# Kernel optimization log

Hardware: AMD Instinct MI355X
Metric: run time of the kernel (lower is better)

The kernel has to match this reference:

```python
import jax, jax.numpy as jnp
import numpy as np
from jax import lax

B, N, NPOINT = 8, 8192, 1024
NSAMPLE = (16, 32)
IN_CH = 64
MLPS = ((64, 64, 128), (64, 96, 128))
EPS = 1e-5


def setup_inputs() -> dict:
    key = jax.random.key(0)
    ks = jax.random.split(key, 16)
    inp = {}
    inp["xyz"] = jax.random.normal(ks[0], (B, 3, N), jnp.float32)
    inp["points"] = jax.random.normal(ks[1], (B, IN_CH, N), jnp.float32)
    ki = 2
    for i, mlp in enumerate(MLPS):
        last = IN_CH + 3
        for j, out in enumerate(mlp):
            inp["w%d_%d" % (i, j)] = jax.random.normal(ks[ki], (out, last), jnp.float32) * (1.0 / float(np.sqrt(last)))
            inp["b%d_%d" % (i, j)] = jnp.zeros((out,), jnp.float32)
            inp["g%d_%d" % (i, j)] = jnp.ones((out,), jnp.float32)
            inp["be%d_%d" % (i, j)] = jnp.zeros((out,), jnp.float32)
            ki += 1
            last = out
    return inp


def _fps(xyz_t):
    # farthest point sampling; xyz_t: [B, N, 3] -> [B, NPOINT] int32
    Bb, Nn, _ = xyz_t.shape

    def step(carry, _):
        dist, far = carry
        c = jnp.take_along_axis(xyz_t, far[:, None, None], axis=1)  # [B,1,3]
        d = jnp.sum((xyz_t - c) ** 2, -1)
        dist = jnp.minimum(dist, d)
        return (dist, jnp.argmax(dist, -1).astype(jnp.int32)), far

    init = (jnp.full((Bb, Nn), 1e10, jnp.float32), jnp.zeros((Bb,), jnp.int32))
    _, cent = lax.scan(step, init, None, length=NPOINT)
    return cent.T  # [B, NPOINT]


def _gather(p, idx):
    # p: [B, N, C], idx: [B, ...] -> [B, ..., C]
    return jax.vmap(lambda a, i: a[i])(p, idx)


def _sqdist(a, b):
    # a: [B, S, 3], b: [B, N, 3] -> [B, S, N] squared euclidean distance
    return (jnp.sum(a * a, -1)[:, :, None] + jnp.sum(b * b, -1)[:, None, :]
            - 2.0 * jnp.einsum('bsc,bnc->bsn', a, b))


def _mlp(x, params):
    # x: [B, C, S, K]; 1x1 Conv2d + BatchNorm2d (batch stats, training mode) + ReLU
    for w, b, g, be in params:
        x = jnp.einsum('oc,bcsk->bosk', w, x) + b[None, :, None, None]
        m = x.mean((0, 2, 3), keepdims=True)
        v = x.var((0, 2, 3), keepdims=True)
        x = (x - m) * lax.rsqrt(v + EPS) * g[None, :, None, None] + be[None, :, None, None]
        x = jax.nn.relu(x)
    return x


def _forward(xyz, points, params):
    xyz_t = jnp.transpose(xyz, (0, 2, 1))     # [B, N, 3]
    pts_t = jnp.transpose(points, (0, 2, 1))  # [B, N, C]
    fps_idx = _fps(xyz_t)
    new_xyz = _gather(xyz_t, fps_idx)         # [B, S, 3]
    outs = []
    for i, k in enumerate(NSAMPLE):
        d = _sqdist(new_xyz, xyz_t)           # [B, S, N]
        _, idx = lax.top_k(-d, k)             # k nearest neighbors
        g_xyz = _gather(xyz_t, idx) - new_xyz[:, :, None, :]  # [B, S, k, 3]
        g_pts = _gather(pts_t, idx)                           # [B, S, k, C]
        feat = jnp.transpose(jnp.concatenate([g_xyz, g_pts], -1), (0, 3, 1, 2))  # [B, 3+C, S, k]
        outs.append(jnp.max(_mlp(feat, params[i]), -1))       # [B, C_out, S]
    return jnp.transpose(new_xyz, (0, 2, 1)), jnp.concatenate(outs, 1)


def reference(xyz, points, w0_0, b0_0, g0_0, be0_0, w0_1, b0_1, g0_1, be0_1, w0_2, b0_2, g0_2, be0_2, w1_0, b1_0, g1_0, be1_0, w1_1, b1_1, g1_1, be1_1, w1_2, b1_2, g1_2, be1_2):
    params = [[(w0_0, b0_0, g0_0, be0_0), (w0_1, b0_1, g0_1, be0_1), (w0_2, b0_2, g0_2, be0_2)],
              [(w1_0, b1_0, g1_0, be1_0), (w1_1, b1_1, g1_1, be1_1), (w1_2, b1_2, g1_2, be1_2)]]
    return _forward(xyz, points, params)
```

## Files before the change

### kernel.cpp

```cpp
#include <hip/hip_runtime.h>
#include <math.h>

#define BN_EPS 1e-5f
constexpr int Bc = 8, Nc = 8192, Sc = 1024, CINc = 64;

typedef float v2f __attribute__((ext_vector_type(2)));

template <int CTRL, int RMASK>
__device__ __forceinline__ unsigned long long dpp_maxu64(unsigned long long k) {
  int lo = (int)(unsigned)k, hi = (int)(unsigned)(k >> 32);
  int olo = __builtin_amdgcn_update_dpp(lo, lo, CTRL, RMASK, 0xF, false);
  int ohi = __builtin_amdgcn_update_dpp(hi, hi, CTRL, RMASK, 0xF, false);
  unsigned long long ok = ((unsigned long long)(unsigned)ohi << 32) | (unsigned)olo;
  return ok > k ? ok : k;
}
template <int CTRL, int RMASK>
__device__ __forceinline__ v2f dpp_sumstep2(v2f v) {
  int olo = __builtin_amdgcn_update_dpp(0, __float_as_int(v.x), CTRL, RMASK, 0xF, false);
  int ohi = __builtin_amdgcn_update_dpp(0, __float_as_int(v.y), CTRL, RMASK, 0xF, false);
  v2f o = {__int_as_float(olo), __int_as_float(ohi)};
  return v + o;
}
__device__ __forceinline__ v2f dpp_sum64v2(v2f v) {
  v = dpp_sumstep2<0x111, 0xF>(v);
  v = dpp_sumstep2<0x112, 0xF>(v);
  v = dpp_sumstep2<0x114, 0xF>(v);
  v = dpp_sumstep2<0x118, 0xF>(v);
  v = dpp_sumstep2<0x142, 0xA>(v);
  v = dpp_sumstep2<0x143, 0xC>(v);
  return v;
}
template <int CTRL>
__device__ __forceinline__ v2f dpp_pkmax(v2f v) {
  int ox = __builtin_amdgcn_update_dpp(__float_as_int(v.x), __float_as_int(v.x), CTRL, 0xF, 0xF, false);
  int oy = __builtin_amdgcn_update_dpp(__float_as_int(v.y), __float_as_int(v.y), CTRL, 0xF, 0xF, false);
  v2f o = {__int_as_float(ox), __int_as_float(oy)};
  return __builtin_elementwise_max(v, o);
}
template <int CTRL>
__device__ __forceinline__ v2f dpp_pkmin(v2f v) {
  int ox = __builtin_amdgcn_update_dpp(__float_as_int(v.x), __float_as_int(v.x), CTRL, 0xF, 0xF, false);
  int oy = __builtin_amdgcn_update_dpp(__float_as_int(v.y), __float_as_int(v.y), CTRL, 0xF, 0xF, false);
  v2f o = {__int_as_float(ox), __int_as_float(oy)};
  return __builtin_elementwise_min(v, o);
}

__device__ __forceinline__ void pproj_body(int i, const float* __restrict__ pts,
                                           const float* __restrict__ wl,
                                           const float* __restrict__ bl,
                                           float* __restrict__ P) {
  int b = i >> 13, n = i & 8191;
  const float* pb = pts + (size_t)b * CINc * Nc + n;
  v2f acc[32];
  const v2f* bl2 = (const v2f*)bl;
#pragma unroll
  for (int o2 = 0; o2 < 32; o2++) acc[o2] = bl2[o2];
  for (int c = 0; c < CINc; c++) {
    float xv = pb[(size_t)c * Nc];
    v2f xv2 = {xv, xv};
    const v2f* wr = (const v2f*)(wl + c * 64);
#pragma unroll
    for (int o2 = 0; o2 < 32; o2++) acc[o2] = __builtin_elementwise_fma(wr[o2], xv2, acc[o2]);
  }
  float4* Pn = (float4*)(P + (size_t)i * 64);
#pragma unroll
  for (int o4 = 0; o4 < 16; o4++)
    Pn[o4] = make_float4(acc[2 * o4].x, acc[2 * o4].y, acc[2 * o4 + 1].x, acc[2 * o4 + 1].y);
}

__global__ __launch_bounds__(512) void mega_kernel(const float* __restrict__ xyz,
                                                   const float* __restrict__ pts,
                                                   const float* __restrict__ w00,
                                                   const float* __restrict__ b00,
                                                   const float* __restrict__ w10,
                                                   const float* __restrict__ b10,
                                                   float4* __restrict__ xyzT,
                                                   float4* __restrict__ nx,
                                                   float* __restrict__ out0,
                                                   float* __restrict__ P0,
                                                   float* __restrict__ P1) {
  __shared__ alignas(16) char smemc[102528];
  int bid = blockIdx.x, t = threadIdx.x;
  if (bid < 8) {
    float* xs = (float*)smemc;
    float* ys = xs + Nc;
    float* zs = ys + Nc;
    int* idxs = (int*)(smemc + 98304);
    unsigned long long* red = (unsigned long long*)(smemc + 102400);
    const float* xb = xyz + (size_t)bid * 3 * Nc;
    float px[16], py[16], pz[16], dd[16];
#pragma unroll
    for (int j = 0; j < 16; j++) {
      int n = j * 512 + t;
      float x = xb[n], y = xb[Nc + n], z = xb[2 * Nc + n];
      px[j] = x; py[j] = y; pz[j] = z;
      xs[n] = x; ys[n] = y; zs[n] = z;
      dd[j] = 1e10f;
    }
    int w = t >> 6;
    __syncthreads();
    int curIdx = 0;
    for (int i = 0; i < Sc; i++) {
      float cx = xs[curIdx], cy = ys[curIdx], cz = zs[curIdx];
      if (t == 0) idxs[i] = curIdx;
      float bd = -1.f;
      int bnidx = 0;
#pragma unroll
      for (int j = 0; j < 16; j++) {
        float dx = px[j] - cx, dy = py[j] - cy, dz = pz[j] - cz;
        float d = fmaf(dz, dz, fmaf(dy, dy, dx * dx));
        d = fminf(dd[j], d);
        dd[j] = d;
        if (d > bd) { bd = d; bnidx = j * 512 + t; }
      }
      unsigned long long key =
          ((unsigned long long)__float_as_uint(bd) << 32) | (unsigned)(~bnidx);
      key = dpp_maxu64<0x111, 0xF>(key);
      key = dpp_maxu64<0x112, 0xF>(key);
      key = dpp_maxu64<0x114, 0xF>(key);
      key = dpp_maxu64<0x118, 0xF>(key);
      key = dpp_maxu64<0x142, 0xA>(key);
      key = dpp_maxu64<0x143, 0xC>(key);
      if ((t & 63) == 63) red[(i & 1) * 8 + w] = key;
      __syncthreads();
      const unsigned long long* rr = red + (i & 1) * 8;
      unsigned long long k2 = rr[0];
#pragma unroll
      for (int u = 1; u < 8; u++) {
        unsigned long long o = rr[u];
        k2 = (o > k2) ? o : k2;
      }
      curIdx = (int)(~(unsigned)(k2 & 0xFFFFFFFFull));
    }
    __syncthreads();
    for (int i2 = t; i2 < Sc; i2 += 512) {
      int idx = idxs[i2];
      float x = xs[idx], y = ys[idx], z = zs[idx];
      nx[bid * Sc + i2] = make_float4(x, y, z, fmaf(z, z, fmaf(y, y, x * x)));
      float* ob = out0 + (size_t)bid * 3 * Sc;
      ob[i2] = x; ob[Sc + i2] = y; ob[2 * Sc + i2] = z;
    }
  } else if (bid < 136) {
    int i = (bid - 8) * 512 + t;
    int b = i >> 13, n = i & 8191;
    const float* xb = xyz + (size_t)b * 3 * Nc;
    float x = xb[n], y = xb[Nc + n], z = xb[2 * Nc + n];
    xyzT[i] = make_float4(x, y, z, fmaf(z, z, fmaf(y, y, x * x)));
  } else {
    bool second = bid >= 264;
    const float* ww = second ? w10 : w00;
    const float* bb = second ? b10 : b00;
    float* PP = second ? P1 : P0;
    float* wl = (float*)smemc;
    float* bl = wl + 64 * 64;
    for (int i2 = t; i2 < 64 * 64; i2 += 512) {
      int c = i2 >> 6, o = i2 & 63;
      wl[i2] = ww[o * 67 + 3 + c];
    }
    if (t < 64) bl[t] = bb[t];
    __syncthreads();
    pproj_body(((bid - (second ? 264 : 136)) * 512) + t, pts, wl, bl, PP);
  }
}

__global__ __launch_bounds__(256) void knn_kernel(const float4* __restrict__ xyzT,
                                                  const float4* __restrict__ newxyz,
                                                  int* __restrict__ knn) {
  int lane = threadIdx.x & 63;
  int sub = lane >> 5;
  int l32 = lane & 31;
  int waveId = blockIdx.x * 4 + (threadIdx.x >> 6);
  int q = waveId * 2 + sub;
  int b = q >> 10;
  float4 qv = newxyz[q];
  const float4* pb = xyzT + (size_t)b * Nc;
  unsigned long long lk = ~0ull;
  unsigned long long worst = ~0ull;
  for (int t0 = 0; t0 < Nc; t0 += 32) {
    float4 p = pb[t0 + l32];
    float dot = fmaf(qv.z, p.z, fmaf(qv.y, p.y, qv.x * p.x));
    float d = fmaf(-2.f, dot, qv.w + p.w);
    unsigned fu = __float_as_uint(d);
    fu ^= (unsigned)(-(int)(fu >> 31)) | 0x80000000u;
    unsigned long long ck = ((unsigned long long)fu << 32) | (unsigned)(t0 + l32);
    unsigned long long bal = __ballot(ck < worst);
    unsigned mymask = (unsigned)(bal >> (sub * 32));
    while (mymask) {
      int src = __ffs(mymask) - 1;
      unsigned long long ckb = __shfl(ck, src, 32);
      unsigned long long bel = __ballot(lk < ckb);
      int cnt = __popc((unsigned)(bel >> (sub * 32)));
      unsigned long long up = __shfl_up(lk, 1, 32);
      lk = (l32 == cnt) ? ckb : ((l32 > cnt) ? up : lk);
      worst = __shfl(lk, 31, 32);
      mymask &= ~(1u << src);
      unsigned long long bal2 = __ballot(ck < worst);
      mymask &= (unsigned)(bal2 >> (sub * 32));
    }
  }
  knn[(size_t)q * 32 + l32] = (int)(lk & 0xFFFFFFFFu);
}

template <int K>
__device__ __forceinline__ void conv1_body(char* smemc, int bidl,
                                           const float4* __restrict__ xyzT,
                                           const float4* __restrict__ nx,
                                           const int* __restrict__ knn,
                                           const float* __restrict__ P,
                                           const float* __restrict__ w0,
                                           float* __restrict__ y,
                                           float* __restrict__ part, int Pos) {
  v2f* wst = (v2f*)smemc;
  float* wx = (float*)(smemc + 8192);
  float* wy = wx + 64;
  float* wz = wy + 64;
  if (threadIdx.x < 64) {
    int o = threadIdx.x;
    wx[o] = w0[o * 67];
    wy[o] = w0[o * 67 + 1];
    wz[o] = w0[o * 67 + 2];
  }
  __syncthreads();
  int gp = bidl * 256 + threadIdx.x;
  int b = gp / Pos, r = gp % Pos;
  int s = r / K, kk = r & (K - 1);
  int n = knn[((size_t)(b * Sc + s)) * 32 + kk];
  float4 c4 = nx[b * Sc + s];
  float4 p4 = xyzT[(size_t)b * Nc + n];
  v2f dx2 = {p4.x - c4.x, p4.x - c4.x};
  v2f dy2 = {p4.y - c4.y, p4.y - c4.y};
  v2f dz2 = {p4.z - c4.z, p4.z - c4.z};
  const float4* Pn = (const float4*)(P + ((size_t)b * Nc + n) * 64);
  v2f acc[32];
#pragma unroll
  for (int o4 = 0; o4 < 16; o4++) {
    float4 v = Pn[o4];
    acc[2 * o4] = (v2f){v.x, v.y};
    acc[2 * o4 + 1] = (v2f){v.z, v.w};
  }
  const v2f* wx2 = (const v2f*)wx;
  const v2f* wy2 = (const v2f*)wy;
  const v2f* wz2 = (const v2f*)wz;
#pragma unroll
  for (int o2 = 0; o2 < 32; o2++) acc[o2] = __builtin_elementwise_fma(wx2[o2], dx2, acc[o2]);
#pragma unroll
  for (int o2 = 0; o2 < 32; o2++) acc[o2] = __builtin_elementwise_fma(wy2[o2], dy2, acc[o2]);
#pragma unroll
  for (int o2 = 0; o2 < 32; o2++) acc[o2] = __builtin_elementwise_fma(wz2[o2], dz2, acc[o2]);
  float4* yb = (float4*)(y + ((size_t)b * Pos + r) * 64);
#pragma unroll
  for (int o4 = 0; o4 < 16; o4++)
    yb[o4] = make_float4(acc[2 * o4].x, acc[2 * o4].y, acc[2 * o4 + 1].x, acc[2 * o4 + 1].y);
  int lane = threadIdx.x & 63, w = threadIdx.x >> 6;
  int row = w * 4 + (lane >> 4);
  bool lead = (lane & 15) == 15;
#pragma unroll
  for (int o2 = 0; o2 < 32; o2++) {
    float v0 = acc[o2].x, v1 = acc[o2].y;
    v2f s0 = (v2f){v0, v0 * v0};
    s0 = dpp_sumstep2<0x111, 0xF>(s0);
    s0 = dpp_sumstep2<0x112, 0xF>(s0);
    s0 = dpp_sumstep2<0x114, 0xF>(s0);
    s0 = dpp_sumstep2<0x118, 0xF>(s0);
    v2f s1 = (v2f){v1, v1 * v1};
    s1 = dpp_sumstep2<0x111, 0xF>(s1);
    s1 = dpp_sumstep2<0x112, 0xF>(s1);
    s1 = dpp_sumstep2<0x114, 0xF>(s1);
    s1 = dpp_sumstep2<0x118, 0xF>(s1);
    if (lead) { wst[row * 64 + 2 * o2] = s0; wst[row * 64 + 2 * o2 + 1] = s1; }
  }
  __syncthreads();
  if (threadIdx.x < 64) {
    int o = threadIdx.x;
    v2f sv = (v2f){0.f, 0.f};
#pragma unroll
    for (int rr = 0; rr < 16; rr++) sv += wst[rr * 64 + o];
    ((v2f*)part)[(size_t)bidl * 64 + o] = sv;
  }
}

__global__ __launch_bounds__(256) void conv1M_kernel(
    const float4* xyzT, const float4* nx, const int* knn,
    const float* P0, const float* w0a, float* y0a, float* part0, int Pos0,
    const float* P1, const float* w0b, float* y0b, float* part1, int Pos1, int split) {
  __shared__ alignas(16) char smemc[8960];
  if ((int)blockIdx.x < split)
    conv1_body<16>(smemc, blockIdx.x, xyzT, nx, knn, P0, w0a, y0a, part0, Pos0);
  else
    conv1_body<32>(smemc, blockIdx.x - split, xyzT, nx, knn, P1, w0b, y0b, part1, Pos1);
}

__global__ __launch_bounds__(256) void bnfinM_kernel(
    const float* part0, const float* g0, const float* be0, float* bn0, int C0, int nblk0, float inv0,
    const float* part1, const float* g1, const float* be1, float* bn1, int C1, int nblk1, float inv1,
    int split) {
  const float* part; const float* g; const float* be; float* bn;
  int C, nblk, c; float invcnt;
  if ((int)blockIdx.x < split) {
    part = part0; g = g0; be = be0; bn = bn0; C = C0; nblk = nblk0; invcnt = inv0; c = blockIdx.x;
  } else {
    part = part1; g = g1; be = be1; bn = bn1; C = C1; nblk = nblk1; invcnt = inv1; c = blockIdx.x - split;
  }
  v2f sq = (v2f){0.f, 0.f};
  for (int i = threadIdx.x; i < nblk; i += 256) sq += ((const v2f*)part)[(size_t)i * C + c];
  sq = dpp_sum64v2(sq);
  __shared__ v2f ls[4];
  int w = threadIdx.x >> 6;
  if ((threadIdx.x & 63) == 63) ls[w] = sq;
  __syncthreads();
  if (threadIdx.x == 0) {
    v2f tt = ls[0] + ls[1] + ls[2] + ls[3];
    float m = tt.x * invcnt;
    float v = tt.y * invcnt - m * m;
    float sc = g[c] / sqrtf(v + BN_EPS);
    bn[c * 2] = sc;
    bn[c * 2 + 1] = fmaf(-m, sc, be[c]);
  }
}

template <int CI, int CO, int K>
__device__ __forceinline__ void convB_body(char* smemc, int bidl,
                                           const float* __restrict__ yin,
                                           const float* __restrict__ wt,
                                           const float* __restrict__ bb,
                                           const float* __restrict__ bn,
                                           float* __restrict__ yout,
                                           float* __restrict__ ymax,
                                           float* __restrict__ ymin,
                                           float* __restrict__ part, int Pos) {
  constexpr int COq = CO / 4;
  constexpr int COq2 = COq / 2;
  float* wl = (float*)smemc;
  float* bnl = wl + CI * CO;
  float* bl = bnl + 2 * CI;
  for (int i = threadIdx.x; i < CI * CO; i += 256) {
    int c = i / CO, o = i % CO;
    wl[i] = wt[o * CI + c];
  }
  for (int i = threadIdx.x; i < 2 * CI; i += 256) bnl[i] = bn[i];
  if (threadIdx.x < CO) bl[threadIdx.x] = bb[threadIdx.x];
  __syncthreads();
  int w = threadIdx.x >> 6, l = threadIdx.x & 63;
  int cb = w * COq;
  int bpb = Pos / 256;
  int b = bidl / bpb;
  int r0 = (bidl % bpb) * 256 + l * 4;
  const float* xin = yin + ((size_t)b * Pos + r0) * CI;
  v2f acc[4][COq2];
#pragma unroll
  for (int p = 0; p < 4; p++)
#pragma unroll
    for (int q = 0; q < COq2; q++) acc[p][q] = ((const v2f*)(bl + cb))[q];
  float4 cur[4], nxt[4];
#pragma unroll
  for (int p = 0; p < 4; p++) cur[p] = ((const float4*)(xin + p * CI))[0];
  for (int ch = 0; ch < CI; ch += 4) {
    if (ch + 4 < CI) {
#pragma unroll
      for (int p = 0; p < 4; p++) nxt[p] = ((const float4*)(xin + p * CI))[(ch >> 2) + 1];
    }
#pragma unroll
    for (int cc = 0; cc < 4; cc++) {
      int c = ch + cc;
      float scv = bnl[2 * c], shv = bnl[2 * c + 1];
      float xv0 = fmaxf(fmaf(((const float*)&cur[0])[cc], scv, shv), 0.f);
      float xv1 = fmaxf(fmaf(((const float*)&cur[1])[cc], scv, shv), 0.f);
      float xv2 = fmaxf(fmaf(((const float*)&cur[2])[cc], scv, shv), 0.f);
      float xv3 = fmaxf(fmaf(((const float*)&cur[3])[cc], scv, shv), 0.f);
      v2f x0 = {xv0, xv0}, x1 = {xv1, xv1}, x2 = {xv2, xv2}, x3 = {xv3, xv3};
      const float4* wr = (const float4*)(wl + c * CO + cb);
#pragma unroll
      for (int o4 = 0; o4 < COq / 4; o4++) {
        float4 wv = wr[o4];
        v2f w01 = {wv.x, wv.y}, w23 = {wv.z, wv.w};
        acc[0][2 * o4] = __builtin_elementwise_fma(w01, x0, acc[0][2 * o4]);
        acc[0][2 * o4 + 1] = __builtin_elementwise_fma(w23, x0, acc[0][2 * o4 + 1]);
        acc[1][2 * o4] = __builtin_elementwise_fma(w01, x1, acc[1][2 * o4]);
        acc[1][2 * o4 + 1] = __builtin_elementwise_fma(w23, x1, acc[1][2 * o4 + 1]);
        acc[2][2 * o4] = __builtin_elementwise_fma(w01, x2, acc[2][2 * o4]);
        acc[2][2 * o4 + 1] = __builtin_elementwise_fma(w23, x2, acc[2][2 * o4 + 1]);
        acc[3][2 * o4] = __builtin_elementwise_fma(w01, x3, acc[3][2 * o4]);
        acc[3][2 * o4 + 1] = __builtin_elementwise_fma(w23, x3, acc[3][2 * o4 + 1]);
      }
    }
#pragma unroll
    for (int p = 0; p < 4; p++) cur[p] = nxt[p];
  }
  if (K == 0) {
#pragma unroll
    for (int p = 0; p < 4; p++) {
      float4* yo = (float4*)(yout + ((size_t)b * Pos + r0 + p) * CO + cb);
#pragma unroll
      for (int o4 = 0; o4 < COq / 4; o4++)
        yo[o4] = make_float4(acc[p][2 * o4].x, acc[p][2 * o4].y, acc[p][2 * o4 + 1].x,
                             acc[p][2 * o4 + 1].y);
    }
  } else {
    int s = r0 / K;
    bool wrt = (K == 16) ? ((l & 3) == 3) : ((l & 7) == 7);
#pragma unroll
    for (int q = 0; q < COq2; q++) {
      v2f mx = __builtin_elementwise_max(__builtin_elementwise_max(acc[0][q], acc[1][q]),
                                         __builtin_elementwise_max(acc[2][q], acc[3][q]));
      v2f mn = __builtin_elementwise_min(__builtin_elementwise_min(acc[0][q], acc[1][q]),
                                         __builtin_elementwise_min(acc[2][q], acc[3][q]));
      mx = dpp_pkmax<0x111>(mx);
      mx = dpp_pkmax<0x112>(mx);
      if (K == 32) mx = dpp_pkmax<0x114>(mx);
      mn = dpp_pkmin<0x111>(mn);
      mn = dpp_pkmin<0x112>(mn);
      if (K == 32) mn = dpp_pkmin<0x114>(mn);
      if (wrt) {
        ymax[((size_t)b * CO + cb + 2 * q) * Sc + s] = mx.x;
        ymax[((size_t)b * CO + cb + 2 * q + 1) * Sc + s] = mx.y;
        ymin[((size_t)b * CO + cb + 2 * q) * Sc + s] = mn.x;
        ymin[((size_t)b * CO + cb + 2 * q + 1) * Sc + s] = mn.y;
      }
    }
  }
#pragma unroll
  for (int q = 0; q < COq2; q++) {
    v2f sv = acc[0][q] + acc[1][q] + acc[2][q] + acc[3][q];
    v2f sq = acc[0][q] * acc[0][q];
    sq = __builtin_elementwise_fma(acc[1][q], acc[1][q], sq);
    sq = __builtin_elementwise_fma(acc[2][q], acc[2][q], sq);
    sq = __builtin_elementwise_fma(acc[3][q], acc[3][q], sq);
    sv = dpp_sum64v2(sv);
    sq = dpp_sum64v2(sq);
    if (l == 63) {
      ((v2f*)part)[(size_t)bidl * CO + cb + 2 * q] = (v2f){sv.x, sq.x};
      ((v2f*)part)[(size_t)bidl * CO + cb + 2 * q + 1] = (v2f){sv.y, sq.y};
    }
  }
}

__global__ __launch_bounds__(256) void conv2M_kernel(
    const float* y0a, const float* w1a, const float* b1a, const float* bn1a, float* y1a,
    float* part0, int Pos0,
    const float* y0b, const float* w1b, const float* b1b, const float* bn1b, float* y1b,
    float* part1, int Pos1, int split) {
  __shared__ alignas(16) char smemc[25472];
  if ((int)blockIdx.x < split)
    convB_body<64, 64, 0>(smemc, blockIdx.x, y0a, w1a, b1a, bn1a, y1a, nullptr, nullptr, part0, Pos0);
  else
    convB_body<64, 96, 0>(smemc, blockIdx.x - split, y0b, w1b, b1b, bn1b, y1b, nullptr, nullptr, part1, Pos1);
}

__global__ __launch_bounds__(256) void conv3M_kernel(
    const float* y1a, const float* w2a, const float* b2a, const float* bn2a, float* ymax0,
    float* ymin0, float* part0, int Pos0,
    const float* y1b, const float* w2b, const float* b2b, const float* bn2b, float* ymax1,
    float* ymin1, float* part1, int Pos1, int split) {
  __shared__ alignas(16) char smemc[50432];
  if ((int)blockIdx.x < split)
    convB_body<64, 128, 16>(smemc, blockIdx.x, y1a, w2a, b2a, bn2a, nullptr, ymax0, ymin0, part0, Pos0);
  else
    convB_body<96, 128, 32>(smemc, blockIdx.x - split, y1b, w2b, b2b, bn2b, nullptr, ymax1, ymin1, part1, Pos1);
}

__global__ __launch_bounds__(256) void bnfin3fM_kernel(
    const float* part0, const float* g0, const float* be0, const float* ymax0,
    const float* ymin0, int nblk0, float inv0, int coff0,
    const float* part1, const float* g1, const float* be1, const float* ymax1,
    const float* ymin1, int nblk1, float inv1, int coff1,
    float* out1, int split) {
  constexpr int C = 128;
  const float* part; const float* g; const float* be; const float* ymaxp; const float* yminp;
  int nblk, c, coff; float invcnt;
  if ((int)blockIdx.x < split) {
    part = part0; g = g0; be = be0; ymaxp = ymax0; yminp = ymin0;
    nblk = nblk0; invcnt = inv0; coff = coff0; c = blockIdx.x;
  } else {
    part = part1; g = g1; be = be1; ymaxp = ymax1; yminp = ymin1;
    nblk = nblk1; invcnt = inv1; coff = coff1; c = blockIdx.x - split;
  }
  v2f sq = (v2f){0.f, 0.f};
  for (int i = threadIdx.x; i < nblk; i += 256) sq += ((const v2f*)part)[(size_t)i * C + c];
  sq = dpp_sum64v2(sq);
  __shared__ v2f ls[4];
  __shared__ float bnc[2];
  int w = threadIdx.x >> 6;
  if ((threadIdx.x & 63) == 63) ls[w] = sq;
  __syncthreads();
  if (threadIdx.x == 0) {
    v2f tt = ls[0] + ls[1] + ls[2] + ls[3];
    float m = tt.x * invcnt;
    float v = tt.y * invcnt - m * m;
    float sc = g[c] / sqrtf(v + BN_EPS);
    bnc[0] = sc;
    bnc[1] = fmaf(-m, sc, be[c]);
  }
  __syncthreads();
  float sc = bnc[0], sh = bnc[1];
  const float* src = (sc >= 0.f) ? ymaxp : yminp;
#pragma unroll
  for (int k = 0; k < 32; k++) {
    int i = k * 256 + threadIdx.x;
    int b = i >> 10, s = i & 1023;
    float v = src[((size_t)b * C + c) * Sc + s];
    out1[((size_t)b * 256 + coff + c) * Sc + s] = fmaxf(fmaf(v, sc, sh), 0.f);
  }
}

extern "C" void kernel_launch(void* const* d_in, const int* in_sizes, int n_in,
                              void* d_out, int out_size, void* d_ws, size_t ws_size,
                              hipStream_t stream) {
  const float* xyz = (const float*)d_in[0];
  const float* pts = (const float*)d_in[1];
  float* ws = (float*)d_ws;
  float* out0 = (float*)d_out;
  float* out1 = out0 + Bc * 3 * Sc;

  float4* xyzT = (float4*)(ws + 0);
  float4* nx = (float4*)(ws + 262144);
  int* knnp = (int*)(ws + 294912);
  float* P0 = ws + 557056;

  const float* d2 = (const float*)d_in[2];
  const float* d3 = (const float*)d_in[3];
  const float* d4 = (const float*)d_in[4];
  const float* d5 = (const float*)d_in[5];
  const float* d6 = (const float*)d_in[6];
  const float* d7 = (const float*)d_in[7];
  const float* d8 = (const float*)d_in[8];
  const float* d9 = (const float*)d_in[9];
  const float* d10 = (const float*)d_in[10];
  const float* d11 = (const float*)d_in[11];
  const float* d12 = (const float*)d_in[12];
  const float* d13 = (const float*)d_in[13];
  const float* d14 = (const float*)d_in[14];
  const float* d15 = (const float*)d_in[15];
  const float* d16 = (const float*)d_in[16];
  const float* d17 = (const float*)d_in[17];
  const float* d18 = (const float*)d_in[18];
  const float* d19 = (const float*)d_in[19];
  const float* d20 = (const float*)d_in[20];
  const float* d21 = (const float*)d_in[21];
  const float* d22 = (const float*)d_in[22];
  const float* d23 = (const float*)d_in[23];
  const float* d24 = (const float*)d_in[24];
  const float* d25 = (const float*)d_in[25];

  float inv0 = 1.f / (float)(Bc * 16384);
  float inv1 = 1.f / (float)(Bc * 32768);

  bool merged = ws_size >= (size_t)72254464 * 4;
  if (merged) {
    float* P1 = ws + 4751360;
    float* y00 = ws + 8945664;
    float* y01 = ws + 17334272;
    float* y10 = ws + 34111488;
    float* y11 = ws + 42500096;
    float* ymax0 = ws + 67665920;
    float* ymin0 = ws + 68714496;
    float* ymax1 = ws + 69763072;
    float* ymin1 = ws + 70811648;
    float* part0 = ws + 71860224;
    float* part1 = ws + 71991296;
    float* bns = ws + 72253440;
    float* bn10 = bns, *bn11 = bns + 256, *bn20 = bns + 512, *bn21 = bns + 768;

    mega_kernel<<<392, 512, 0, stream>>>(xyz, pts, d2, d3, d14, d15, xyzT, nx, out0, P0, P1);
    knn_kernel<<<1024, 256, 0, stream>>>(xyzT, nx, knnp);
    conv1M_kernel<<<1536, 256, 0, stream>>>(xyzT, nx, knnp, P0, d2, y00, part0, 16384, P1, d14,
                                            y01, part1, 32768, 512);
    bnfinM_kernel<<<128, 256, 0, stream>>>(part0, d4, d5, bn10, 64, 512, inv0, part1, d16, d17,
                                           bn11, 64, 1024, inv1, 64);
    conv2M_kernel<<<1536, 256, 0, stream>>>(y00, d6, d7, bn10, y10, part0, 16384, y01, d18, d19,
                                            bn11, y11, part1, 32768, 512);
    bnfinM_kernel<<<160, 256, 0, stream>>>(part0, d8, d9, bn20, 64, 512, inv0, part1, d20, d21,
                                           bn21, 96, 1024, inv1, 64);
    conv3M_kernel<<<1536, 256, 0, stream>>>(y10, d10, d11, bn20, ymax0, ymin0, part0, 16384, y11,
                                            d22, d23, bn21, ymax1, ymin1, part1, 32768, 512);
    bnfin3fM_kernel<<<256, 256, 0, stream>>>(part0, d12, d13, ymax0, ymin0, 512, inv0, 0, part1,
                                             d24, d25, ymax1, ymin1, 1024, inv1, 128, out1, 128);
  } else {
    float* y0 = ws + 4751360;
    float* y1 = ws + 21528576;
    float* P1 = ws + 29917184;
    float* ymax = ws + 46694400;
    float* ymin = ws + 47742976;
    float* part = ws + 48791552;
    float* bn1 = ws + 49053696;
    float* bn2 = ws + 49053824;

    mega_kernel<<<392, 512, 0, stream>>>(xyz, pts, d2, d3, d14, d15, xyzT, nx, out0, P0, P1);
    knn_kernel<<<1024, 256, 0, stream>>>(xyzT, nx, knnp);

    conv1M_kernel<<<512, 256, 0, stream>>>(xyzT, nx, knnp, P0, d2, y0, part, 16384, P0, d2, y0,
                                           part, 16384, 512);
    bnfinM_kernel<<<64, 256, 0, stream>>>(part, d4, d5, bn1, 64, 512, inv0, part, d4, d5, bn1, 64,
                                          512, inv0, 64);
    conv2M_kernel<<<512, 256, 0, stream>>>(y0, d6, d7, bn1, y1, part, 16384, y0, d6, d7, bn1, y1,
                                           part, 16384, 512);
    bnfinM_kernel<<<64, 256, 0, stream>>>(part, d8, d9, bn2, 64, 512, inv0, part, d8, d9, bn2, 64,
                                          512, inv0, 64);
    conv3M_kernel<<<512, 256, 0, stream>>>(y1, d10, d11, bn2, ymax, ymin, part, 16384, y1, d10,
                                           d11, bn2, ymax, ymin, part, 16384, 512);
    bnfin3fM_kernel<<<128, 256, 0, stream>>>(part, d12, d13, ymax, ymin, 512, inv0, 0, part, d12,
                                             d13, ymax, ymin, 512, inv0, 0, out1, 128);

    conv1M_kernel<<<1024, 256, 0, stream>>>(xyzT, nx, knnp, P1, d14, y0, part, 32768, P1, d14, y0,
                                            part, 32768, 0);
    bnfinM_kernel<<<64, 256, 0, stream>>>(part, d16, d17, bn1, 64, 1024, inv1, part, d16, d17,
                                          bn1, 64, 1024, inv1, 0);
    conv2M_kernel<<<1024, 256, 0, stream>>>(y0, d18, d19, bn1, y1, part, 32768, y0, d18, d19, bn1,
                                            y1, part, 32768, 0);
    bnfinM_kernel<<<96, 256, 0, stream>>>(part, d20, d21, bn2, 96, 1024, inv1, part, d20, d21,
                                          bn2, 96, 1024, inv1, 0);
    conv3M_kernel<<<1024, 256, 0, stream>>>(y1, d22, d23, bn2, ymax, ymin, part, 32768, y1, d22,
                                            d23, bn2, ymax, ymin, part, 32768, 0);
    bnfin3fM_kernel<<<128, 256, 0, stream>>>(part, d24, d25, ymax, ymin, 1024, inv1, 128, part,
                                             d24, d25, ymax, ymin, 1024, inv1, 128, out1, 0);
  }
  (void)in_sizes; (void)n_in; (void)out_size; (void)ws_size;
}
```

Measured before the change: 1.387 ms.

## Store intermediate activations channel-major per block tile for coalesced access

Intermediate MLP activations change from row-major [pos][channel] to a per-256-position block tile in channel-major order, [block][channel][256]. The first-layer writer and the conv layers' reader and writer all switch to this layout. Each lane's per-channel load and store become contiguous across the wavefront, replacing strided float4 accesses with a stride of CI floats. The risk is that the layout is now tied to blocks of 256 positions: every producer and consumer must agree on it, and the reader now issues one float4 load per channel instead of per four channels.

```diff
diff --git a/kernel.cpp b/kernel.cpp
--- a/kernel.cpp
+++ b/kernel.cpp
@@ -247,10 +247,12 @@
   for (int o2 = 0; o2 < 32; o2++) acc[o2] = __builtin_elementwise_fma(wy2[o2], dy2, acc[o2]);
 #pragma unroll
   for (int o2 = 0; o2 < 32; o2++) acc[o2] = __builtin_elementwise_fma(wz2[o2], dz2, acc[o2]);
-  float4* yb = (float4*)(y + ((size_t)b * Pos + r) * 64);
-#pragma unroll
-  for (int o4 = 0; o4 < 16; o4++)
-    yb[o4] = make_float4(acc[2 * o4].x, acc[2 * o4].y, acc[2 * o4 + 1].x, acc[2 * o4 + 1].y);
+  float* yt = y + (size_t)bidl * 64 * 256 + threadIdx.x;
+#pragma unroll
+  for (int o2 = 0; o2 < 32; o2++) {
+    yt[(size_t)(2 * o2) * 256] = acc[o2].x;
+    yt[(size_t)(2 * o2 + 1) * 256] = acc[o2].y;
+  }
   int lane = threadIdx.x & 63, w = threadIdx.x >> 6;
   int row = w * 4 + (lane >> 4);
   bool lead = (lane & 15) == 15;
@@ -345,55 +347,45 @@
   int bpb = Pos / 256;
   int b = bidl / bpb;
   int r0 = (bidl % bpb) * 256 + l * 4;
-  const float* xin = yin + ((size_t)b * Pos + r0) * CI;
+  const float4* xt = (const float4*)(yin + (size_t)bidl * CI * 256) + l;
   v2f acc[4][COq2];
 #pragma unroll
   for (int p = 0; p < 4; p++)
 #pragma unroll
     for (int q = 0; q < COq2; q++) acc[p][q] = ((const v2f*)(bl + cb))[q];
-  float4 cur[4], nxt[4];
-#pragma unroll
-  for (int p = 0; p < 4; p++) cur[p] = ((const float4*)(xin + p * CI))[0];
-  for (int ch = 0; ch < CI; ch += 4) {
-    if (ch + 4 < CI) {
-#pragma unroll
-      for (int p = 0; p < 4; p++) nxt[p] = ((const float4*)(xin + p * CI))[(ch >> 2) + 1];
-    }
-#pragma unroll
-    for (int cc = 0; cc < 4; cc++) {
-      int c = ch + cc;
-      float scv = bnl[2 * c], shv = bnl[2 * c + 1];
-      float xv0 = fmaxf(fmaf(((const float*)&cur[0])[cc], scv, shv), 0.f);
-      float xv1 = fmaxf(fmaf(((const float*)&cur[1])[cc], scv, shv), 0.f);
-      float xv2 = fmaxf(fmaf(((const float*)&cur[2])[cc], scv, shv), 0.f);
-      float xv3 = fmaxf(fmaf(((const float*)&cur[3])[cc], scv, shv), 0.f);
-      v2f x0 = {xv0, xv0}, x1 = {xv1, xv1}, x2 = {xv2, xv2}, x3 = {xv3, xv3};
-      const float4* wr = (const float4*)(wl + c * CO + cb);
-#pragma unroll
-      for (int o4 = 0; o4 < COq / 4; o4++) {
-        float4 wv = wr[o4];
-        v2f w01 = {wv.x, wv.y}, w23 = {wv.z, wv.w};
-        acc[0][2 * o4] = __builtin_elementwise_fma(w01, x0, acc[0][2 * o4]);
-        acc[0][2 * o4 + 1] = __builtin_elementwise_fma(w23, x0, acc[0][2 * o4 + 1]);
-        acc[1][2 * o4] = __builtin_elementwise_fma(w01, x1, acc[1][2 * o4]);
-        acc[1][2 * o4 + 1] = __builtin_elementwise_fma(w23, x1, acc[1][2 * o4 + 1]);
-        acc[2][2 * o4] = __builtin_elementwise_fma(w01, x2, acc[2][2 * o4]);
-        acc[2][2 * o4 + 1] = __builtin_elementwise_fma(w23, x2, acc[2][2 * o4 + 1]);
-        acc[3][2 * o4] = __builtin_elementwise_fma(w01, x3, acc[3][2 * o4]);
-        acc[3][2 * o4 + 1] = __builtin_elementwise_fma(w23, x3, acc[3][2 * o4 + 1]);
-      }
-    }
-#pragma unroll
-    for (int p = 0; p < 4; p++) cur[p] = nxt[p];
+  float4 cur = xt[0], nxt;
+  for (int c = 0; c < CI; c++) {
+    if (c + 1 < CI) nxt = xt[(c + 1) * 64];
+    float scv = bnl[2 * c], shv = bnl[2 * c + 1];
+    float xv0 = fmaxf(fmaf(cur.x, scv, shv), 0.f);
+    float xv1 = fmaxf(fmaf(cur.y, scv, shv), 0.f);
+    float xv2 = fmaxf(fmaf(cur.z, scv, shv), 0.f);
+    float xv3 = fmaxf(fmaf(cur.w, scv, shv), 0.f);
+    v2f x0 = {xv0, xv0}, x1 = {xv1, xv1}, x2 = {xv2, xv2}, x3 = {xv3, xv3};
+    const float4* wr = (const float4*)(wl + c * CO + cb);
+#pragma unroll
+    for (int o4 = 0; o4 < COq / 4; o4++) {
+      float4 wv = wr[o4];
+      v2f w01 = {wv.x, wv.y}, w23 = {wv.z, wv.w};
+      acc[0][2 * o4] = __builtin_elementwise_fma(w01, x0, acc[0][2 * o4]);
+      acc[0][2 * o4 + 1] = __builtin_elementwise_fma(w23, x0, acc[0][2 * o4 + 1]);
+      acc[1][2 * o4] = __builtin_elementwise_fma(w01, x1, acc[1][2 * o4]);
+      acc[1][2 * o4 + 1] = __builtin_elementwise_fma(w23, x1, acc[1][2 * o4 + 1]);
+      acc[2][2 * o4] = __builtin_elementwise_fma(w01, x2, acc[2][2 * o4]);
+      acc[2][2 * o4 + 1] = __builtin_elementwise_fma(w23, x2, acc[2][2 * o4 + 1]);
+      acc[3][2 * o4] = __builtin_elementwise_fma(w01, x3, acc[3][2 * o4]);
+      acc[3][2 * o4 + 1] = __builtin_elementwise_fma(w23, x3, acc[3][2 * o4 + 1]);
+    }
+    cur = nxt;
   }
   if (K == 0) {
-#pragma unroll
-    for (int p = 0; p < 4; p++) {
-      float4* yo = (float4*)(yout + ((size_t)b * Pos + r0 + p) * CO + cb);
-#pragma unroll
-      for (int o4 = 0; o4 < COq / 4; o4++)
-        yo[o4] = make_float4(acc[p][2 * o4].x, acc[p][2 * o4].y, acc[p][2 * o4 + 1].x,
-                             acc[p][2 * o4 + 1].y);
+    float* yo = yout + (size_t)bidl * CO * 256;
+#pragma unroll
+    for (int q = 0; q < COq2; q++) {
+      ((float4*)(yo + (size_t)(cb + 2 * q) * 256))[l] =
+          make_float4(acc[0][q].x, acc[1][q].x, acc[2][q].x, acc[3][q].x);
+      ((float4*)(yo + (size_t)(cb + 2 * q + 1) * 256))[l] =
+          make_float4(acc[0][q].y, acc[1][q].y, acc[2][q].y, acc[3][q].y);
     }
   } else {
     int s = r0 / K;
```

Result: faster. 1.298 ms (-6.4%).
